# Performance work log

Measured on AMD Instinct MI355X. Metric: run time of the kernel, lower is better.

## Reference

```python
import jax, jax.numpy as jnp
import numpy as np

N_NODES = 50000
N_EDGES = 800000
IN_DIM = 512
HEADS = 4
HID = 64
OUT = 64
NEG_SLOPE = 0.2  # DGL GATConv default


def gat_layer(x, W, attn_l, attn_r, bias, src, dst, n_nodes, heads, d_out):
    # x: [N, F_in], W: [F_in, heads*d_out], attn_l/attn_r: [heads, d_out], bias: [heads, d_out]
    f = (x @ W).reshape(n_nodes, heads, d_out)          # [N, H, D]
    el = jnp.sum(f * attn_l, axis=-1)                   # [N, H]
    er = jnp.sum(f * attn_r, axis=-1)                   # [N, H]
    e = jax.nn.leaky_relu(el[src] + er[dst], NEG_SLOPE) # [E, H]
    # segment softmax over incoming edges of each dst node
    m = jax.ops.segment_max(e, dst, num_segments=n_nodes)       # [N, H]
    ex = jnp.exp(e - m[dst])                                     # [E, H]
    den = jax.ops.segment_sum(ex, dst, num_segments=n_nodes)    # [N, H]
    a = ex / den[dst]                                            # [E, H]
    # scatter-aggregate weighted messages
    out = jax.ops.segment_sum(a[:, :, None] * f[src], dst, num_segments=n_nodes)  # [N, H, D]
    return out + bias, a


def setup_inputs() -> dict:
    key = jax.random.key(0)
    ks = jax.random.split(key, 12)
    features = jax.random.normal(ks[0], (N_NODES, IN_DIM), dtype=jnp.float32)
    src = jax.random.randint(ks[1], (N_EDGES,), 0, N_NODES, dtype=jnp.int32)
    dst = jax.random.randint(ks[2], (N_EDGES,), 0, N_NODES, dtype=jnp.int32)
    s1 = 1.0 / np.sqrt(IN_DIM)
    s2 = 1.0 / np.sqrt(HEADS * HID)
    W1 = jax.random.normal(ks[3], (IN_DIM, HEADS * HID), dtype=jnp.float32) * s1
    al1 = jax.random.normal(ks[4], (HEADS, HID), dtype=jnp.float32) * s1
    ar1 = jax.random.normal(ks[5], (HEADS, HID), dtype=jnp.float32) * s1
    b1 = jnp.zeros((HEADS, HID), dtype=jnp.float32)
    W2 = jax.random.normal(ks[6], (HEADS * HID, OUT), dtype=jnp.float32) * s2
    al2 = jax.random.normal(ks[7], (1, OUT), dtype=jnp.float32) * s2
    ar2 = jax.random.normal(ks[8], (1, OUT), dtype=jnp.float32) * s2
    b2 = jnp.zeros((1, OUT), dtype=jnp.float32)
    return {"features": features, "W1": W1, "al1": al1, "ar1": ar1, "b1": b1,
            "W2": W2, "al2": al2, "ar2": ar2, "b2": b2, "src": src, "dst": dst}


def reference(features, W1, al1, ar1, b1, W2, al2, ar2, b2, src, dst):
    h1, _ = gat_layer(features, W1, al1, ar1, b1, src, dst, N_NODES, HEADS, HID)
    h1 = jax.nn.elu(h1.reshape(N_NODES, HEADS * HID))   # flatten heads + ELU
    h2, _ = gat_layer(h1, W2, al2, ar2, b2, src, dst, N_NODES, 1, OUT)
    return h2  # [N, 1, OUT]
```

## Files before the change

kernel.cpp:

```cpp
#include <hip/hip_runtime.h>

#define N_NODES 50000
#define N_EDGES 800000
#define IN_DIM 512
#define NEG_SLOPE 0.2f

typedef short short8 __attribute__((ext_vector_type(8)));
typedef float f32x16 __attribute__((ext_vector_type(16)));
typedef __attribute__((address_space(3))) unsigned int lds_u32;
typedef const __attribute__((address_space(1))) unsigned int glb_u32;

__device__ __forceinline__ unsigned bf16rne(float f) {
  union { float f; unsigned u; } v;
  v.f = f;
  return (v.u + 0x7FFFu + ((v.u >> 16) & 1u)) >> 16;
}
__device__ __forceinline__ void tsplit8(float4 a, float4 b, short8& hi,
                                        short8& lo) {
  float fa[8] = {a.x, a.y, a.z, a.w, b.x, b.y, b.z, b.w};
#pragma unroll
  for (int i = 0; i < 8; i++) {
    unsigned u = __float_as_uint(fa[i]);
    hi[i] = (short)(u >> 16);
    float lof = fa[i] - __uint_as_float(u & 0xffff0000u);
    lo[i] = (short)(__float_as_uint(lof) >> 16);
  }
}

__global__ void pack_w(const float* __restrict__ W, short* __restrict__ Bhi,
                       int N) {
  int k = blockIdx.x, n = threadIdx.x;
  float w = W[(size_t)k * N + n];
  int ksub = k >> 4, kh = (k >> 3) & 1, j = k & 7;
  int nsub = n >> 5, lane2 = (n & 31) | (kh << 5);
  size_t off = (((size_t)ksub * (N >> 5) + nsub) * 64 + lane2) * 8 + j;
  Bhi[off] = (short)bf16rne(w);
}

template <int K, int NSUBS, int NTILES>
__global__ __launch_bounds__(256) void gemm_mfma(
    const float* __restrict__ A, const short* __restrict__ Bhi_,
    unsigned short* __restrict__ Cb, const float* __restrict__ alv,
    const float* __restrict__ arv, float* __restrict__ el,
    float* __restrict__ er, int M) {
  constexpr int N = NSUBS * 32;
  constexpr int MT = 4 / NTILES;
  constexpr int BROWS = MT * 32;
  constexpr int T = K / 32;
  constexpr int GB = NSUBS / 2;
  constexpr int BSTEP_S = NSUBS * 1024;
  static_assert(MT + GB == 5, "vmcnt literals assume 5 loads/wave/step");
  __shared__ float ldsA[2][BROWS * 32];
  __shared__ short ldsB[2][BSTEP_S];

  const int tid = threadIdx.x;
  const int lane = tid & 63;
  const int w = tid >> 6;
  const int l31 = lane & 31;
  const int half = lane >> 5;
  const int local_mt = w / NTILES;
  const int ntile = w % NTILES;
  const int block_row0 = blockIdx.x * BROWS;

  const float* gsrcA[MT];
#pragma unroll
  for (int q = 0; q < MT; q++) {
    int seg = w * MT + q;
    int r = seg * 8 + (lane >> 3);
    int c = (lane & 7) ^ (r & 7);
    int grow = block_row0 + r;
    if (grow > M - 1) grow = M - 1;
    gsrcA[q] = A + (size_t)grow * K + c * 4;
  }
  const short* bsrc = Bhi_ + lane * 8;

  const int arow = local_mt * 32 + l31;
  const int rs = arow & 7;

  f32x16 acc0 = {}, acc1 = {};

  auto STAGE = [&](int b, int t) {
#pragma unroll
    for (int q = 0; q < MT; q++) {
      __builtin_amdgcn_global_load_lds((glb_u32*)(gsrcA[q] + t * 32),
                                       (lds_u32*)&ldsA[b][(w * MT + q) * 256],
                                       16, 0, 0);
    }
#pragma unroll
    for (int j = 0; j < GB; j++) {
      __builtin_amdgcn_global_load_lds(
          (glb_u32*)(bsrc + (size_t)t * BSTEP_S + (w * GB + j) * 512),
          (lds_u32*)&ldsB[b][(w * GB + j) * 512], 16, 0, 0);
    }
  };

  STAGE(0, 0);

  int buf = 0;
  for (int t = 0; t < T; t++) {
    if (t + 1 < T) {
      STAGE(buf ^ 1, t + 1);
      asm volatile("s_waitcnt vmcnt(5)" ::: "memory");
    } else {
      asm volatile("s_waitcnt vmcnt(0)" ::: "memory");
    }
    __builtin_amdgcn_s_barrier();

    const float* lA = ldsA[buf];
    const short* lB = ldsB[buf];
#pragma unroll
    for (int u = 0; u < 2; u++) {
      short8 cb0 = *(const short8*)&lB[(u * NSUBS + ntile * 2) * 512 + lane * 8];
      short8 cb1 =
          *(const short8*)&lB[(u * NSUBS + ntile * 2 + 1) * 512 + lane * 8];
      int c0 = u * 4 + half * 2;
      float4 a0 = *(const float4*)&lA[arow * 32 + (c0 ^ rs) * 4];
      float4 a1 = *(const float4*)&lA[arow * 32 + ((c0 + 1) ^ rs) * 4];
      short8 ah, al8;
      tsplit8(a0, a1, ah, al8);
      acc0 = __builtin_amdgcn_mfma_f32_32x32x16_bf16(ah, cb0, acc0, 0, 0, 0);
      acc0 = __builtin_amdgcn_mfma_f32_32x32x16_bf16(al8, cb0, acc0, 0, 0, 0);
      acc1 = __builtin_amdgcn_mfma_f32_32x32x16_bf16(ah, cb1, acc1, 0, 0, 0);
      acc1 = __builtin_amdgcn_mfma_f32_32x32x16_bf16(al8, cb1, acc1, 0, 0, 0);
    }
    asm volatile("s_waitcnt lgkmcnt(0)" ::: "memory");
    __builtin_amdgcn_s_barrier();
    buf ^= 1;
  }

  int colbase = ntile * 64 + l31;
  float wa0 = alv[colbase], wa1 = alv[colbase + 32];
  float wr0 = arv[colbase], wr1 = arv[colbase + 32];
  const int mrow0 = block_row0 + local_mt * 32;
#pragma unroll
  for (int r = 0; r < 16; r++) {
    int roff = (r & 3) + 8 * (r >> 2) + 4 * half;
    int row = mrow0 + roff;
    if (row < M) {
      Cb[(size_t)row * N + colbase] = (unsigned short)bf16rne(acc0[r]);
      Cb[(size_t)row * N + colbase + 32] = (unsigned short)bf16rne(acc1[r]);
    }
    float elv = acc0[r] * wa0 + acc1[r] * wa1;
    float erv = acc0[r] * wr0 + acc1[r] * wr1;
#pragma unroll
    for (int off = 1; off < 32; off <<= 1) {
      elv += __shfl_xor(elv, off);
      erv += __shfl_xor(erv, off);
    }
    if (l31 == 0 && row < M) {
      el[row * NTILES + ntile] = elv;
      er[row * NTILES + ntile] = erv;
    }
  }
}

__global__ void hist_kernel(const int* __restrict__ dst,
                            int* __restrict__ counts) {
  int e = blockIdx.x * blockDim.x + threadIdx.x;
  if (e < N_EDGES) atomicAdd(&counts[dst[e]], 1);
}

#define NSCAN 196
__global__ __launch_bounds__(256) void scan_part(const int* __restrict__ counts,
                                                 int* __restrict__ offsets,
                                                 int* __restrict__ bsums) {
  __shared__ int sh[256];
  int t = threadIdx.x;
  int i = blockIdx.x * 256 + t;
  int v = (i < N_NODES) ? counts[i] : 0;
  sh[t] = v;
  __syncthreads();
  for (int o = 1; o < 256; o <<= 1) {
    int x = (t >= o) ? sh[t - o] : 0;
    __syncthreads();
    sh[t] += x;
    __syncthreads();
  }
  if (i < N_NODES) offsets[i] = sh[t] - v;
  if (t == 255) bsums[blockIdx.x] = sh[255];
}
__global__ __launch_bounds__(256) void scan_top(int* __restrict__ bsums) {
  __shared__ int sh[256];
  int t = threadIdx.x;
  int v = (t < NSCAN) ? bsums[t] : 0;
  sh[t] = v;
  __syncthreads();
  for (int o = 1; o < 256; o <<= 1) {
    int x = (t >= o) ? sh[t - o] : 0;
    __syncthreads();
    sh[t] += x;
    __syncthreads();
  }
  if (t < NSCAN) bsums[t] = sh[t] - v;
}
__global__ __launch_bounds__(256) void scan_add(int* __restrict__ offsets,
                                                const int* __restrict__ bsums) {
  int i = blockIdx.x * 256 + threadIdx.x;
  if (i < N_NODES) offsets[i] += bsums[blockIdx.x];
  if (i == 0) offsets[N_NODES] = N_EDGES;
}

__global__ void scatter_kernel(const int* __restrict__ src,
                               const int* __restrict__ dst,
                               const int* __restrict__ offsets,
                               int* __restrict__ fill,
                               int* __restrict__ csr_src) {
  int e = blockIdx.x * blockDim.x + threadIdx.x;
  if (e < N_EDGES) {
    int d = dst[e];
    int pos = offsets[d] + atomicAdd(&fill[d], 1);
    csr_src[pos] = src[e];
  }
}

__global__ __launch_bounds__(256) void agg1_kernel(
    const int* __restrict__ offsets, const int* __restrict__ csr_src,
    const float* __restrict__ el, const float* __restrict__ er,
    const unsigned short* __restrict__ fb, const float* __restrict__ bias,
    float* __restrict__ h1) {
  __shared__ float red[3][256];
  __shared__ float dred[3][32];
  int n = blockIdx.x;
  int t = threadIdx.x;
  int w = t >> 6, lane = t & 63;
  int l31 = lane & 31;
  int eslot = lane >> 5;
  int h = l31 >> 3;
  int slot = w * 2 + eslot;
  int off0 = offsets[n], deg = offsets[n + 1] - off0;
  float erh = er[n * 4 + h];
  float4 aLo = {0.f, 0.f, 0.f, 0.f}, aHi = {0.f, 0.f, 0.f, 0.f};
  float4 bLo = {0.f, 0.f, 0.f, 0.f}, bHi = {0.f, 0.f, 0.f, 0.f};
  float sden = 0.f;
  int i = slot;
  for (; i + 8 < deg; i += 16) {
    int s0 = csr_src[off0 + i];
    int s1 = csr_src[off0 + i + 8];
    uint4 p0 = *(const uint4*)(fb + (size_t)s0 * 256 + l31 * 8);
    uint4 p1 = *(const uint4*)(fb + (size_t)s1 * 256 + l31 * 8);
    float e0 = el[s0 * 4 + h] + erh;
    float e1 = el[s1 * 4 + h] + erh;
    e0 = e0 > 0.f ? e0 : NEG_SLOPE * e0;
    e1 = e1 > 0.f ? e1 : NEG_SLOPE * e1;
    float a0 = __expf(e0), a1 = __expf(e1);
    sden += a0 + a1;
    aLo.x += a0 * __uint_as_float(p0.x << 16);
    aLo.y += a0 * __uint_as_float(p0.x & 0xffff0000u);
    aLo.z += a0 * __uint_as_float(p0.y << 16);
    aLo.w += a0 * __uint_as_float(p0.y & 0xffff0000u);
    aHi.x += a0 * __uint_as_float(p0.z << 16);
    aHi.y += a0 * __uint_as_float(p0.z & 0xffff0000u);
    aHi.z += a0 * __uint_as_float(p0.w << 16);
    aHi.w += a0 * __uint_as_float(p0.w & 0xffff0000u);
    bLo.x += a1 * __uint_as_float(p1.x << 16);
    bLo.y += a1 * __uint_as_float(p1.x & 0xffff0000u);
    bLo.z += a1 * __uint_as_float(p1.y << 16);
    bLo.w += a1 * __uint_as_float(p1.y & 0xffff0000u);
    bHi.x += a1 * __uint_as_float(p1.z << 16);
    bHi.y += a1 * __uint_as_float(p1.z & 0xffff0000u);
    bHi.z += a1 * __uint_as_float(p1.w << 16);
    bHi.w += a1 * __uint_as_float(p1.w & 0xffff0000u);
  }
  if (i < deg) {
    int s0 = csr_src[off0 + i];
    uint4 p0 = *(const uint4*)(fb + (size_t)s0 * 256 + l31 * 8);
    float e0 = el[s0 * 4 + h] + erh;
    e0 = e0 > 0.f ? e0 : NEG_SLOPE * e0;
    float a0 = __expf(e0);
    sden += a0;
    aLo.x += a0 * __uint_as_float(p0.x << 16);
    aLo.y += a0 * __uint_as_float(p0.x & 0xffff0000u);
    aLo.z += a0 * __uint_as_float(p0.y << 16);
    aLo.w += a0 * __uint_as_float(p0.y & 0xffff0000u);
    aHi.x += a0 * __uint_as_float(p0.z << 16);
    aHi.y += a0 * __uint_as_float(p0.z & 0xffff0000u);
    aHi.z += a0 * __uint_as_float(p0.w << 16);
    aHi.w += a0 * __uint_as_float(p0.w & 0xffff0000u);
  }
  aLo.x += bLo.x; aLo.y += bLo.y; aLo.z += bLo.z; aLo.w += bLo.w;
  aHi.x += bHi.x; aHi.y += bHi.y; aHi.z += bHi.z; aHi.w += bHi.w;
  aLo.x += __shfl_xor(aLo.x, 32);
  aLo.y += __shfl_xor(aLo.y, 32);
  aLo.z += __shfl_xor(aLo.z, 32);
  aLo.w += __shfl_xor(aLo.w, 32);
  aHi.x += __shfl_xor(aHi.x, 32);
  aHi.y += __shfl_xor(aHi.y, 32);
  aHi.z += __shfl_xor(aHi.z, 32);
  aHi.w += __shfl_xor(aHi.w, 32);
  sden += __shfl_xor(sden, 32);
  if (w && lane < 32) {
    *(float4*)(&red[w - 1][l31 * 8]) = aLo;
    *(float4*)(&red[w - 1][l31 * 8 + 4]) = aHi;
    dred[w - 1][l31] = sden;
  }
  __syncthreads();
  if (w == 0 && lane < 32) {
    float den = sden;
#pragma unroll
    for (int j = 0; j < 3; j++) {
      float4 rL = *(float4*)(&red[j][l31 * 8]);
      float4 rH = *(float4*)(&red[j][l31 * 8 + 4]);
      aLo.x += rL.x; aLo.y += rL.y; aLo.z += rL.z; aLo.w += rL.w;
      aHi.x += rH.x; aHi.y += rH.y; aHi.z += rH.z; aHi.w += rH.w;
      den += dred[j][l31];
    }
    float invd = den > 0.f ? 1.0f / den : 0.f;
    float4 b0 = ((const float4*)bias)[l31 * 2];
    float4 b1 = ((const float4*)bias)[l31 * 2 + 1];
    float o[8] = {aLo.x * invd + b0.x, aLo.y * invd + b0.y,
                  aLo.z * invd + b0.z, aLo.w * invd + b0.w,
                  aHi.x * invd + b1.x, aHi.y * invd + b1.y,
                  aHi.z * invd + b1.z, aHi.w * invd + b1.w};
#pragma unroll
    for (int j = 0; j < 8; j++) o[j] = o[j] > 0.f ? o[j] : __expf(o[j]) - 1.0f;
    float4 o0 = {o[0], o[1], o[2], o[3]};
    float4 o1 = {o[4], o[5], o[6], o[7]};
    *(float4*)(h1 + (size_t)n * 256 + l31 * 8) = o0;
    *(float4*)(h1 + (size_t)n * 256 + l31 * 8 + 4) = o1;
  }
}

__global__ __launch_bounds__(256) void agg2_kernel(
    const int* __restrict__ offsets, const int* __restrict__ csr_src,
    const float* __restrict__ el, const float* __restrict__ er,
    const unsigned short* __restrict__ fb2, const float* __restrict__ bias,
    float* __restrict__ out) {
  int w = threadIdx.x >> 6, lane = threadIdx.x & 63;
  int n = blockIdx.x * 4 + w;
  if (n >= N_NODES) return;
  int dg = lane & 15, eslot = lane >> 4;
  int off0 = offsets[n], deg = offsets[n + 1] - off0;
  float ern = er[n];
  float4 acc = {0.f, 0.f, 0.f, 0.f};
  float4 acc2 = {0.f, 0.f, 0.f, 0.f};
  float sden = 0.f;
  int i = eslot;
  for (; i + 4 < deg; i += 8) {
    int s0 = csr_src[off0 + i];
    int s1 = csr_src[off0 + i + 4];
    uint2 p0 = *(const uint2*)(fb2 + (size_t)s0 * 64 + dg * 4);
    uint2 p1 = *(const uint2*)(fb2 + (size_t)s1 * 64 + dg * 4);
    float e0 = el[s0] + ern;
    float e1 = el[s1] + ern;
    e0 = e0 > 0.f ? e0 : NEG_SLOPE * e0;
    e1 = e1 > 0.f ? e1 : NEG_SLOPE * e1;
    float a0 = __expf(e0), a1 = __expf(e1);
    sden += a0 + a1;
    acc.x += a0 * __uint_as_float(p0.x << 16);
    acc.y += a0 * __uint_as_float(p0.x & 0xffff0000u);
    acc.z += a0 * __uint_as_float(p0.y << 16);
    acc.w += a0 * __uint_as_float(p0.y & 0xffff0000u);
    acc2.x += a1 * __uint_as_float(p1.x << 16);
    acc2.y += a1 * __uint_as_float(p1.x & 0xffff0000u);
    acc2.z += a1 * __uint_as_float(p1.y << 16);
    acc2.w += a1 * __uint_as_float(p1.y & 0xffff0000u);
  }
  if (i < deg) {
    int s0 = csr_src[off0 + i];
    uint2 p0 = *(const uint2*)(fb2 + (size_t)s0 * 64 + dg * 4);
    float e0 = el[s0] + ern;
    e0 = e0 > 0.f ? e0 : NEG_SLOPE * e0;
    float a0 = __expf(e0);
    sden += a0;
    acc.x += a0 * __uint_as_float(p0.x << 16);
    acc.y += a0 * __uint_as_float(p0.x & 0xffff0000u);
    acc.z += a0 * __uint_as_float(p0.y << 16);
    acc.w += a0 * __uint_as_float(p0.y & 0xffff0000u);
  }
  acc.x += acc2.x;
  acc.y += acc2.y;
  acc.z += acc2.z;
  acc.w += acc2.w;
#pragma unroll
  for (int off = 16; off < 64; off <<= 1) {
    acc.x += __shfl_xor(acc.x, off);
    acc.y += __shfl_xor(acc.y, off);
    acc.z += __shfl_xor(acc.z, off);
    acc.w += __shfl_xor(acc.w, off);
    sden += __shfl_xor(sden, off);
  }
  if (eslot == 0) {
    float invd = sden > 0.f ? 1.0f / sden : 0.f;
    float4 b = ((const float4*)bias)[dg];
    float4 ov = {acc.x * invd + b.x, acc.y * invd + b.y, acc.z * invd + b.z,
                 acc.w * invd + b.w};
    *(float4*)(out + (size_t)n * 64 + dg * 4) = ov;
  }
}

extern "C" void kernel_launch(void* const* d_in, const int* in_sizes, int n_in,
                              void* d_out, int out_size, void* d_ws,
                              size_t ws_size, hipStream_t stream) {
  const float* features = (const float*)d_in[0];
  const float* W1 = (const float*)d_in[1];
  const float* al1 = (const float*)d_in[2];
  const float* ar1 = (const float*)d_in[3];
  const float* b1 = (const float*)d_in[4];
  const float* W2 = (const float*)d_in[5];
  const float* al2 = (const float*)d_in[6];
  const float* ar2 = (const float*)d_in[7];
  const float* b2 = (const float*)d_in[8];
  const int* src = (const int*)d_in[9];
  const int* dst = (const int*)d_in[10];
  float* out = (float*)d_out;

  float* h1 = (float*)d_ws;
  unsigned short* fb = (unsigned short*)(h1 + (size_t)N_NODES * 256);
  unsigned short* fb2 = fb;
  float* el1 = (float*)(fb + (size_t)N_NODES * 256);
  float* er1 = el1 + N_NODES * 4;
  float* el2 = er1 + N_NODES * 4;
  float* er2 = el2 + N_NODES;
  int* counts = (int*)(er2 + N_NODES);
  int* offsets = counts + N_NODES;
  int* fill = offsets + N_NODES + 1;
  int* csr_src = fill + N_NODES;
  int* bsums = csr_src + N_EDGES;

  short* b1hi = (short*)d_out;
  short* b2hi = (short*)fill;

  hipMemsetAsync(counts, 0, N_NODES * sizeof(int), stream);
  hipMemsetAsync(fill, 0, N_NODES * sizeof(int), stream);
  hist_kernel<<<(N_EDGES + 255) / 256, 256, 0, stream>>>(dst, counts);
  scan_part<<<NSCAN, 256, 0, stream>>>(counts, offsets, bsums);
  scan_top<<<1, 256, 0, stream>>>(bsums);
  scan_add<<<NSCAN, 256, 0, stream>>>(offsets, bsums);
  scatter_kernel<<<(N_EDGES + 255) / 256, 256, 0, stream>>>(src, dst, offsets,
                                                            fill, csr_src);

  pack_w<<<512, 256, 0, stream>>>(W1, b1hi, 256);
  pack_w<<<256, 64, 0, stream>>>(W2, b2hi, 64);

  gemm_mfma<IN_DIM, 8, 4><<<1563, 256, 0, stream>>>(features, b1hi, fb, al1,
                                                    ar1, el1, er1, N_NODES);
  agg1_kernel<<<N_NODES, 256, 0, stream>>>(offsets, csr_src, el1, er1, fb, b1,
                                           h1);

  gemm_mfma<256, 2, 1><<<391, 256, 0, stream>>>(h1, b2hi, fb2, al2, ar2, el2,
                                                er2, N_NODES);
  agg2_kernel<<<(N_NODES + 3) / 4, 256, 0, stream>>>(offsets, csr_src, el2,
                                                     er2, fb2, b2, out);
}
```

Before: 404.8 us.

## Precompute exp of attention logits per node and widen GEMM tile per wave

The attention score exp(leaky_relu(el+er)) is factored into per-node precomputed exponentials exp(el), exp(0.2*el) (and likewise for er), so the per-edge work becomes two multiplies and a select instead of an add, a compare and an exp. This removes transcendental work from the edge-aggregation loops but doubles the bytes gathered per edge for the logit terms and drops the max-subtraction, so there is some overflow risk. Separately, the first-layer GEMM now has each wave compute four N-subtiles (NTILES=2, 64-row blocks, 782 blocks), which raises B-operand reuse per wave and halves the grid at the cost of more accumulator registers.

After: 417.9 us. +3.3%, slower.

```diff
diff --git a/kernel.cpp b/kernel.cpp
--- a/kernel.cpp
+++ b/kernel.cpp
@@ -41,15 +41,19 @@
 __global__ __launch_bounds__(256) void gemm_mfma(
     const float* __restrict__ A, const short* __restrict__ Bhi_,
     unsigned short* __restrict__ Cb, const float* __restrict__ alv,
-    const float* __restrict__ arv, float* __restrict__ el,
-    float* __restrict__ er, int M) {
+    const float* __restrict__ arv, float2* __restrict__ elt,
+    float2* __restrict__ ert, int M) {
   constexpr int N = NSUBS * 32;
-  constexpr int MT = 4 / NTILES;
-  constexpr int BROWS = MT * 32;
+  constexpr int MTILES = 4 / NTILES;
+  constexpr int BROWS = MTILES * 32;
   constexpr int T = K / 32;
+  constexpr int MT = MTILES;
   constexpr int GB = NSUBS / 2;
+  constexpr int NSUBT = NSUBS / NTILES;
+  constexpr int HPW = NSUBT / 2;
+  constexpr int NHEADS = NSUBS / 2;
   constexpr int BSTEP_S = NSUBS * 1024;
-  static_assert(MT + GB == 5, "vmcnt literals assume 5 loads/wave/step");
+  static_assert(MT + GB == 5 || MT + GB == 6, "vmcnt literal coverage");
   __shared__ float ldsA[2][BROWS * 32];
   __shared__ short ldsB[2][BSTEP_S];
 
@@ -77,7 +81,7 @@
   const int arow = local_mt * 32 + l31;
   const int rs = arow & 7;
 
-  f32x16 acc0 = {}, acc1 = {};
+  f32x16 acc[NSUBT] = {};
 
   auto STAGE = [&](int b, int t) {
 #pragma unroll
@@ -100,7 +104,10 @@
   for (int t = 0; t < T; t++) {
     if (t + 1 < T) {
       STAGE(buf ^ 1, t + 1);
-      asm volatile("s_waitcnt vmcnt(5)" ::: "memory");
+      if constexpr (MT + GB == 5)
+        asm volatile("s_waitcnt vmcnt(5)" ::: "memory");
+      else
+        asm volatile("s_waitcnt vmcnt(6)" ::: "memory");
     } else {
       asm volatile("s_waitcnt vmcnt(0)" ::: "memory");
     }
@@ -110,46 +117,54 @@
     const short* lB = ldsB[buf];
 #pragma unroll
     for (int u = 0; u < 2; u++) {
-      short8 cb0 = *(const short8*)&lB[(u * NSUBS + ntile * 2) * 512 + lane * 8];
-      short8 cb1 =
-          *(const short8*)&lB[(u * NSUBS + ntile * 2 + 1) * 512 + lane * 8];
       int c0 = u * 4 + half * 2;
       float4 a0 = *(const float4*)&lA[arow * 32 + (c0 ^ rs) * 4];
       float4 a1 = *(const float4*)&lA[arow * 32 + ((c0 + 1) ^ rs) * 4];
       short8 ah, al8;
       tsplit8(a0, a1, ah, al8);
-      acc0 = __builtin_amdgcn_mfma_f32_32x32x16_bf16(ah, cb0, acc0, 0, 0, 0);
-      acc0 = __builtin_amdgcn_mfma_f32_32x32x16_bf16(al8, cb0, acc0, 0, 0, 0);
-      acc1 = __builtin_amdgcn_mfma_f32_32x32x16_bf16(ah, cb1, acc1, 0, 0, 0);
-      acc1 = __builtin_amdgcn_mfma_f32_32x32x16_bf16(al8, cb1, acc1, 0, 0, 0);
+#pragma unroll
+      for (int j = 0; j < NSUBT; j++) {
+        short8 cbj = *(const short8*)&lB[(u * NSUBS + ntile * NSUBT + j) * 512 +
+                                         lane * 8];
+        acc[j] = __builtin_amdgcn_mfma_f32_32x32x16_bf16(ah, cbj, acc[j], 0, 0, 0);
+        acc[j] =
+            __builtin_amdgcn_mfma_f32_32x32x16_bf16(al8, cbj, acc[j], 0, 0, 0);
+      }
     }
     asm volatile("s_waitcnt lgkmcnt(0)" ::: "memory");
     __builtin_amdgcn_s_barrier();
     buf ^= 1;
   }
 
-  int colbase = ntile * 64 + l31;
-  float wa0 = alv[colbase], wa1 = alv[colbase + 32];
-  float wr0 = arv[colbase], wr1 = arv[colbase + 32];
   const int mrow0 = block_row0 + local_mt * 32;
 #pragma unroll
-  for (int r = 0; r < 16; r++) {
-    int roff = (r & 3) + 8 * (r >> 2) + 4 * half;
-    int row = mrow0 + roff;
-    if (row < M) {
-      Cb[(size_t)row * N + colbase] = (unsigned short)bf16rne(acc0[r]);
-      Cb[(size_t)row * N + colbase + 32] = (unsigned short)bf16rne(acc1[r]);
-    }
-    float elv = acc0[r] * wa0 + acc1[r] * wa1;
-    float erv = acc0[r] * wr0 + acc1[r] * wr1;
-#pragma unroll
-    for (int off = 1; off < 32; off <<= 1) {
-      elv += __shfl_xor(elv, off);
-      erv += __shfl_xor(erv, off);
-    }
-    if (l31 == 0 && row < M) {
-      el[row * NTILES + ntile] = elv;
-      er[row * NTILES + ntile] = erv;
+  for (int h = 0; h < HPW; h++) {
+    int c0 = ntile * NSUBT * 32 + 2 * h * 32 + l31;
+    float wa0 = alv[c0], wa1 = alv[c0 + 32];
+    float wr0 = arv[c0], wr1 = arv[c0 + 32];
+#pragma unroll
+    for (int r = 0; r < 16; r++) {
+      int roff = (r & 3) + 8 * (r >> 2) + 4 * half;
+      int row = mrow0 + roff;
+      float v0 = acc[2 * h][r], v1 = acc[2 * h + 1][r];
+      if (row < M) {
+        Cb[(size_t)row * N + c0] = (unsigned short)bf16rne(v0);
+        Cb[(size_t)row * N + c0 + 32] = (unsigned short)bf16rne(v1);
+      }
+      float elv = v0 * wa0 + v1 * wa1;
+      float erv = v0 * wr0 + v1 * wr1;
+#pragma unroll
+      for (int off = 1; off < 32; off <<= 1) {
+        elv += __shfl_xor(elv, off);
+        erv += __shfl_xor(erv, off);
+      }
+      if (l31 == 0 && row < M) {
+        int hg = ntile * HPW + h;
+        elt[(size_t)row * NHEADS + hg] =
+            make_float2(__expf(elv), __expf(NEG_SLOPE * elv));
+        ert[(size_t)row * NHEADS + hg] =
+            make_float2(__expf(erv), __expf(NEG_SLOPE * erv));
+      }
     }
   }
 }
@@ -215,7 +230,7 @@
 
 __global__ __launch_bounds__(256) void agg1_kernel(
     const int* __restrict__ offsets, const int* __restrict__ csr_src,
-    const float* __restrict__ el, const float* __restrict__ er,
+    const float2* __restrict__ elt, const float2* __restrict__ ert,
     const unsigned short* __restrict__ fb, const float* __restrict__ bias,
     float* __restrict__ h1) {
   __shared__ float red[3][256];
@@ -228,7 +243,7 @@
   int h = l31 >> 3;
   int slot = w * 2 + eslot;
   int off0 = offsets[n], deg = offsets[n + 1] - off0;
-  float erh = er[n * 4 + h];
+  float2 fv = ert[n * 4 + h];
   float4 aLo = {0.f, 0.f, 0.f, 0.f}, aHi = {0.f, 0.f, 0.f, 0.f};
   float4 bLo = {0.f, 0.f, 0.f, 0.f}, bHi = {0.f, 0.f, 0.f, 0.f};
   float sden = 0.f;
@@ -238,11 +253,12 @@
     int s1 = csr_src[off0 + i + 8];
     uint4 p0 = *(const uint4*)(fb + (size_t)s0 * 256 + l31 * 8);
     uint4 p1 = *(const uint4*)(fb + (size_t)s1 * 256 + l31 * 8);
-    float e0 = el[s0 * 4 + h] + erh;
-    float e1 = el[s1 * 4 + h] + erh;
-    e0 = e0 > 0.f ? e0 : NEG_SLOPE * e0;
-    e1 = e1 > 0.f ? e1 : NEG_SLOPE * e1;
-    float a0 = __expf(e0), a1 = __expf(e1);
+    float2 q0 = elt[s0 * 4 + h];
+    float2 q1 = elt[s1 * 4 + h];
+    float t10 = q0.x * fv.x, t20 = q0.y * fv.y;
+    float t11 = q1.x * fv.x, t21 = q1.y * fv.y;
+    float a0 = t10 > 1.f ? t10 : t20;
+    float a1 = t11 > 1.f ? t11 : t21;
     sden += a0 + a1;
     aLo.x += a0 * __uint_as_float(p0.x << 16);
     aLo.y += a0 * __uint_as_float(p0.x & 0xffff0000u);
@@ -264,9 +280,9 @@
   if (i < deg) {
     int s0 = csr_src[off0 + i];
     uint4 p0 = *(const uint4*)(fb + (size_t)s0 * 256 + l31 * 8);
-    float e0 = el[s0 * 4 + h] + erh;
-    e0 = e0 > 0.f ? e0 : NEG_SLOPE * e0;
-    float a0 = __expf(e0);
+    float2 q0 = elt[s0 * 4 + h];
+    float t10 = q0.x * fv.x, t20 = q0.y * fv.y;
+    float a0 = t10 > 1.f ? t10 : t20;
     sden += a0;
     aLo.x += a0 * __uint_as_float(p0.x << 16);
     aLo.y += a0 * __uint_as_float(p0.x & 0xffff0000u);
@@ -322,7 +338,7 @@
 
 __global__ __launch_bounds__(256) void agg2_kernel(
     const int* __restrict__ offsets, const int* __restrict__ csr_src,
-    const float* __restrict__ el, const float* __restrict__ er,
+    const float2* __restrict__ elt, const float2* __restrict__ ert,
     const unsigned short* __restrict__ fb2, const float* __restrict__ bias,
     float* __restrict__ out) {
   int w = threadIdx.x >> 6, lane = threadIdx.x & 63;
@@ -330,7 +346,7 @@
   if (n >= N_NODES) return;
   int dg = lane & 15, eslot = lane >> 4;
   int off0 = offsets[n], deg = offsets[n + 1] - off0;
-  float ern = er[n];
+  float2 fv = ert[n];
   float4 acc = {0.f, 0.f, 0.f, 0.f};
   float4 acc2 = {0.f, 0.f, 0.f, 0.f};
   float sden = 0.f;
@@ -340,11 +356,12 @@
     int s1 = csr_src[off0 + i + 4];
     uint2 p0 = *(const uint2*)(fb2 + (size_t)s0 * 64 + dg * 4);
     uint2 p1 = *(const uint2*)(fb2 + (size_t)s1 * 64 + dg * 4);
-    float e0 = el[s0] + ern;
-    float e1 = el[s1] + ern;
-    e0 = e0 > 0.f ? e0 : NEG_SLOPE * e0;
-    e1 = e1 > 0.f ? e1 : NEG_SLOPE * e1;
-    float a0 = __expf(e0), a1 = __expf(e1);
+    float2 q0 = elt[s0];
+    float2 q1 = elt[s1];
+    float t10 = q0.x * fv.x, t20 = q0.y * fv.y;
+    float t11 = q1.x * fv.x, t21 = q1.y * fv.y;
+    float a0 = t10 > 1.f ? t10 : t20;
+    float a1 = t11 > 1.f ? t11 : t21;
     sden += a0 + a1;
     acc.x += a0 * __uint_as_float(p0.x << 16);
     acc.y += a0 * __uint_as_float(p0.x & 0xffff0000u);
@@ -358,9 +375,9 @@
   if (i < deg) {
     int s0 = csr_src[off0 + i];
     uint2 p0 = *(const uint2*)(fb2 + (size_t)s0 * 64 + dg * 4);
-    float e0 = el[s0] + ern;
-    e0 = e0 > 0.f ? e0 : NEG_SLOPE * e0;
-    float a0 = __expf(e0);
+    float2 q0 = elt[s0];
+    float t10 = q0.x * fv.x, t20 = q0.y * fv.y;
+    float a0 = t10 > 1.f ? t10 : t20;
     sden += a0;
     acc.x += a0 * __uint_as_float(p0.x << 16);
     acc.y += a0 * __uint_as_float(p0.x & 0xffff0000u);
@@ -407,11 +424,11 @@
   float* h1 = (float*)d_ws;
   unsigned short* fb = (unsigned short*)(h1 + (size_t)N_NODES * 256);
   unsigned short* fb2 = fb;
-  float* el1 = (float*)(fb + (size_t)N_NODES * 256);
-  float* er1 = el1 + N_NODES * 4;
-  float* el2 = er1 + N_NODES * 4;
-  float* er2 = el2 + N_NODES;
-  int* counts = (int*)(er2 + N_NODES);
+  float2* elt1 = (float2*)(fb + (size_t)N_NODES * 256);
+  float2* ert1 = elt1 + (size_t)N_NODES * 4;
+  float2* elt2 = ert1 + (size_t)N_NODES * 4;
+  float2* ert2 = elt2 + N_NODES;
+  int* counts = (int*)(ert2 + N_NODES);
   int* offsets = counts + N_NODES;
   int* fill = offsets + N_NODES + 1;
   int* csr_src = fill + N_NODES;
@@ -432,13 +449,13 @@
   pack_w<<<512, 256, 0, stream>>>(W1, b1hi, 256);
   pack_w<<<256, 64, 0, stream>>>(W2, b2hi, 64);
 
-  gemm_mfma<IN_DIM, 8, 4><<<1563, 256, 0, stream>>>(features, b1hi, fb, al1,
-                                                    ar1, el1, er1, N_NODES);
-  agg1_kernel<<<N_NODES, 256, 0, stream>>>(offsets, csr_src, el1, er1, fb, b1,
-                                           h1);
-
-  gemm_mfma<256, 2, 1><<<391, 256, 0, stream>>>(h1, b2hi, fb2, al2, ar2, el2,
-                                                er2, N_NODES);
-  agg2_kernel<<<(N_NODES + 3) / 4, 256, 0, stream>>>(offsets, csr_src, el2,
-                                                     er2, fb2, b2, out);
-}
+  gemm_mfma<IN_DIM, 8, 2><<<782, 256, 0, stream>>>(features, b1hi, fb, al1,
+                                                   ar1, elt1, ert1, N_NODES);
+  agg1_kernel<<<N_NODES, 256, 0, stream>>>(offsets, csr_src, elt1, ert1, fb,
+                                           b1, h1);
+
+  gemm_mfma<256, 2, 1><<<391, 256, 0, stream>>>(h1, b2hi, fb2, al2, ar2, elt2,
+                                                ert2, N_NODES);
+  agg2_kernel<<<(N_NODES + 3) / 4, 256, 0, stream>>>(offsets, csr_src, elt2,
+                                                     ert2, fb2, b2, out);
+}
```
